# Performance work log

Measured on AMD Instinct MI355X. Metric: run time of the kernel, lower is better.

Reference implementation:

```python
import jax, jax.numpy as jnp
import numpy as np

D_MODEL = 256
NUM_HEADS = 8
CHUNK = 500
KEY_DIM = D_MODEL // NUM_HEADS      # 32
HEAD_DIM = KEY_DIM                  # value_factor = 1
SCALING = KEY_DIM ** -0.5
B, C, T = 2, 4, 2000                # T must be a multiple of CHUNK


def _rel_pos_constants(slen):
    # RetNetRelPos(chunkwise_recurrent=True)
    angle = 1.0 / (10000.0 ** jnp.linspace(0.0, 1.0, KEY_DIM // 2))
    angle = jnp.repeat(angle, 2)                                     # (KEY_DIM,)
    decay = jnp.log(1.0 - 2.0 ** (-5.0 - jnp.arange(NUM_HEADS, dtype=jnp.float32)))
    idx = jnp.arange(slen, dtype=jnp.float32)
    sin = jnp.sin(idx[:, None] * angle[None, :])                     # (T, KEY_DIM)
    cos = jnp.cos(idx[:, None] * angle[None, :])
    bi = jnp.arange(CHUNK, dtype=jnp.float32)
    diff = bi[:, None] - bi[None, :]
    mask = jnp.where(diff >= 0, jnp.exp(decay[:, None, None] * diff), 0.0)  # (H, cs, cs)
    last_row_sum = mask[:, -1].sum(-1)                               # (H,)
    value_inner_decay = (mask[:, -1] / last_row_sum[:, None])[:, :, None]   # (H, cs, 1)
    scale = jnp.sqrt(mask.sum(-1, keepdims=True))                    # (H, cs, 1)
    inner_mask = mask / scale
    cross_decay = jnp.exp(decay * CHUNK)[:, None, None]              # (H, 1, 1)
    qid = jnp.exp(decay[:, None] * (bi + 1.0))[:, :, None]           # (H, cs, 1)
    query_inner_decay = qid / (scale / last_row_sum[:, None, None])
    return sin, cos, inner_mask, cross_decay, query_inner_decay, value_inner_decay


def _rotate_every_two(x):
    x1, x2 = x[..., ::2], x[..., 1::2]
    return jnp.stack((-x2, x1), axis=-1).reshape(x.shape)


def _theta_shift(x, sin, cos):
    return x * cos + _rotate_every_two(x) * sin


def _layer_norm(x, g, b, eps=1e-5):
    mu = x.mean(-1, keepdims=True)
    var = ((x - mu) ** 2).mean(-1, keepdims=True)
    return (x - mu) * jax.lax.rsqrt(var + eps) * g + b


def _retention(x, qw, kw, vw, gw, ow):
    # MultiScaleRetention, chunkwise-recurrent mode
    bsz, t, _ = x.shape
    sin, cos, mask, cross_decay, q_decay, v_decay = _rel_pos_constants(t)
    q = x @ qw.T
    k = (x @ kw.T) * SCALING
    v = x @ vw.T
    g = x @ gw.T
    q = q.reshape(bsz, t, NUM_HEADS, KEY_DIM).transpose(0, 2, 1, 3)
    k = k.reshape(bsz, t, NUM_HEADS, KEY_DIM).transpose(0, 2, 1, 3)
    qr = _theta_shift(q, sin, cos)
    kr = _theta_shift(k, sin, cos)
    nc = t // CHUNK
    qr = qr.reshape(bsz, NUM_HEADS, nc, CHUNK, KEY_DIM).transpose(0, 2, 1, 3, 4)
    kr = kr.reshape(bsz, NUM_HEADS, nc, CHUNK, KEY_DIM).transpose(0, 2, 1, 3, 4)
    v = v.reshape(bsz, nc, CHUNK, NUM_HEADS, HEAD_DIM).transpose(0, 1, 3, 2, 4)
    qk = jnp.einsum('bnhik,bnhjk->bnhij', qr, kr) * mask             # (b,nc,h,cs,cs)
    inner_scale = jnp.maximum(jax.lax.stop_gradient(jnp.abs(qk)).sum(-1, keepdims=True), 1.0)
    inner_out = (qk / inner_scale) @ v                               # (b,nc,h,cs,hd)
    kv = jnp.einsum('bnhjk,bnhjd->bnhkd', kr, v * v_decay)           # (b,nc,h,kd,hd)

    def step(carry, kv_i):
        kv_state, kv_scale = carry
        out = (kv_state / kv_scale, kv_scale)
        kv_state = kv_state * cross_decay + kv_i
        kv_scale = jnp.maximum(
            jax.lax.stop_gradient(jnp.abs(kv_state)).sum(-2, keepdims=True).max(-1, keepdims=True), 1.0)
        return (kv_state, kv_scale), out

    init = (jnp.zeros((bsz, NUM_HEADS, KEY_DIM, HEAD_DIM), v.dtype),
            jnp.ones((bsz, NUM_HEADS, 1, 1), v.dtype))
    _, (kv_rec, cross_scale) = jax.lax.scan(step, init, jnp.moveaxis(kv, 1, 0))
    kv_rec = jnp.moveaxis(kv_rec, 0, 1)                              # (b,nc,h,kd,hd)
    cross_scale = jnp.moveaxis(cross_scale, 0, 1)                    # (b,nc,h,1,1)
    all_scale = jnp.maximum(inner_scale, cross_scale)
    cross_out = jnp.einsum('bnhik,bnhkd->bnhid', qr * q_decay, kv_rec)
    out = inner_out / (all_scale / inner_scale) + cross_out / (all_scale / cross_scale)
    out = out.transpose(0, 1, 3, 2, 4)                               # (b,nc,cs,h,hd)
    # group_norm = RMSNorm(head_dim, eps=1e-6, no affine)
    out = out * jax.lax.rsqrt(jnp.mean(out ** 2, -1, keepdims=True) + 1e-6)
    out = out.reshape(bsz, t, NUM_HEADS * HEAD_DIM)
    return (jax.nn.silu(g) * out) @ ow.T


def _mha(x, in_w, in_b, out_w, out_b):
    # torch.nn.MultiheadAttention, batch_first, eval (dropout off)
    bsz, s, _ = x.shape
    hd = D_MODEL // NUM_HEADS
    qkv = x @ in_w.T + in_b
    q, k, v = jnp.split(qkv, 3, axis=-1)
    q = q.reshape(bsz, s, NUM_HEADS, hd).transpose(0, 2, 1, 3) * (hd ** -0.5)
    k = k.reshape(bsz, s, NUM_HEADS, hd).transpose(0, 2, 1, 3)
    v = v.reshape(bsz, s, NUM_HEADS, hd).transpose(0, 2, 1, 3)
    attn = jax.nn.softmax(jnp.einsum('bhqd,bhkd->bhqk', q, k), axis=-1)
    out = jnp.einsum('bhqk,bhkd->bhqd', attn, v).transpose(0, 2, 1, 3).reshape(bsz, s, D_MODEL)
    return out @ out_w.T + out_b


def setup_inputs() -> dict:
    key = jax.random.key(0)
    ks = jax.random.split(key, 10)
    s = D_MODEL ** -0.5
    return {
        'inputs': jax.random.normal(ks[0], (B, C, T, D_MODEL), jnp.float32),
        'ln1_g': jnp.ones((D_MODEL,), jnp.float32),
        'ln1_b': jnp.zeros((D_MODEL,), jnp.float32),
        'ln2_g': jnp.ones((D_MODEL,), jnp.float32),
        'ln2_b': jnp.zeros((D_MODEL,), jnp.float32),
        'qw': jax.random.normal(ks[1], (D_MODEL, D_MODEL), jnp.float32) * s,
        'kw': jax.random.normal(ks[2], (D_MODEL, D_MODEL), jnp.float32) * s,
        'vw': jax.random.normal(ks[3], (D_MODEL, D_MODEL), jnp.float32) * s,
        'gw': jax.random.normal(ks[4], (D_MODEL, D_MODEL), jnp.float32) * s,
        'ow': jax.random.normal(ks[5], (D_MODEL, D_MODEL), jnp.float32) * s,
        'in_w': jax.random.normal(ks[6], (3 * D_MODEL, D_MODEL), jnp.float32) * s,
        'in_b': jnp.zeros((3 * D_MODEL,), jnp.float32),
        'out_w': jax.random.normal(ks[7], (D_MODEL, D_MODEL), jnp.float32) * s,
        'out_b': jnp.zeros((D_MODEL,), jnp.float32),
    }


def reference(inputs, ln1_g, ln1_b, ln2_g, ln2_b, qw, kw, vw, gw, ow, in_w, in_b, out_w, out_b):
    Bb, Cc, Tt, Dd = inputs.shape
    x = inputs.reshape(Bb * Cc, Tt, Dd)
    x = x + _retention(_layer_norm(x, ln1_g, ln1_b), qw, kw, vw, gw, ow)
    x = x.reshape(Bb, Cc, Tt, Dd).transpose(0, 2, 1, 3).reshape(Bb * Tt, Cc, Dd)
    x = x + _mha(_layer_norm(x, ln2_g, ln2_b), in_w, in_b, out_w, out_b)
    return x.reshape(Bb, Tt, Cc, Dd).transpose(0, 2, 1, 3)
```

## Files before the change

### kernel.cpp

```cpp
#include <hip/hip_runtime.h>
#include <math.h>

#define TLEN 2000
#define NSEQ 8
#define NHEADS 8
#define KD 32
#define CHUNKN 500
#define NCHUNK 4
#define MROWS 16000
#define SCALING 0.1767766952966369f

typedef float f32x4 __attribute__((ext_vector_type(4)));
typedef short s16x8 __attribute__((ext_vector_type(8)));
typedef unsigned short u16x8 __attribute__((ext_vector_type(8)));
typedef unsigned short u16x4 __attribute__((ext_vector_type(4)));

__device__ __forceinline__ unsigned short f2bf(float f) {
    unsigned int u = __float_as_uint(f);
    unsigned int r = (u + 0x7FFFu + ((u >> 16) & 1u)) >> 16;
    return (unsigned short)r;
}
__device__ __forceinline__ float bf2f(unsigned short h) {
    return __uint_as_float(((unsigned int)h) << 16);
}
__device__ __forceinline__ unsigned int cvtpk(float lo, float hi) {
    unsigned int r;
    asm("v_cvt_pk_bf16_f32 %0, %1, %2" : "=v"(r) : "v"(lo), "v"(hi));
    return r;
}

__global__ __launch_bounds__(256) void tab_kernel(float* __restrict__ sinT,
                                                  float* __restrict__ cosT) {
    int idx = blockIdx.x * 256 + threadIdx.x;
    if (idx >= TLEN * 16) return;
    int t = idx >> 4, a = idx & 15;
    float ang = powf(10000.0f, -(float)a / 15.0f);
    float th = (float)t * ang;
    sinT[idx] = sinf(th);
    cosT[idx] = cosf(th);
}

__global__ __launch_bounds__(256) void wcast_kernel(
    const float* __restrict__ qw, const float* __restrict__ kw,
    const float* __restrict__ vw, const float* __restrict__ gw,
    const float* __restrict__ ow, const float* __restrict__ inw,
    const float* __restrict__ outw, unsigned short* __restrict__ W) {
    int i = blockIdx.x * 1024 + threadIdx.x * 4;
    const float* src; int off;
    if (i < 65536)       { src = qw;   off = i; }
    else if (i < 131072) { src = kw;   off = i - 65536; }
    else if (i < 196608) { src = vw;   off = i - 131072; }
    else if (i < 262144) { src = gw;   off = i - 196608; }
    else if (i < 327680) { src = ow;   off = i - 262144; }
    else if (i < 524288) { src = inw;  off = i - 327680; }
    else                 { src = outw; off = i - 524288; }
    float4 v = *(const float4*)(src + off);
    u16x4 o;
    o[0] = f2bf(v.x); o[1] = f2bf(v.y); o[2] = f2bf(v.z); o[3] = f2bf(v.w);
    *(u16x4*)(W + i) = o;
}

__global__ __launch_bounds__(256) void ln_kernel(const float* __restrict__ x,
                                                 const float* __restrict__ gam,
                                                 const float* __restrict__ bet,
                                                 unsigned short* __restrict__ H,
                                                 unsigned short* __restrict__ L,
                                                 int rows) {
    int wid = threadIdx.x >> 6, lane = threadIdx.x & 63;
    int row = blockIdx.x * 4 + wid;
    if (row >= rows) return;
    const float* xr = x + (size_t)row * 256;
    float4 v = *(const float4*)(xr + lane * 4);
    float s = v.x + v.y + v.z + v.w;
    #pragma unroll
    for (int o = 32; o; o >>= 1) s += __shfl_xor(s, o);
    float mu = s * (1.0f / 256.0f);
    float dx = v.x - mu, dy = v.y - mu, dz = v.z - mu, dw = v.w - mu;
    float ss = dx * dx + dy * dy + dz * dz + dw * dw;
    #pragma unroll
    for (int o = 32; o; o >>= 1) ss += __shfl_xor(ss, o);
    float rstd = rsqrtf(ss * (1.0f / 256.0f) + 1e-5f);
    float4 g4 = *(const float4*)(gam + lane * 4);
    float4 b4 = *(const float4*)(bet + lane * 4);
    float ov[4];
    ov[0] = dx * rstd * g4.x + b4.x;
    ov[1] = dy * rstd * g4.y + b4.y;
    ov[2] = dz * rstd * g4.z + b4.z;
    ov[3] = dw * rstd * g4.w + b4.w;
    u16x4 hv, lv;
    #pragma unroll
    for (int j = 0; j < 4; ++j) {
        hv[j] = f2bf(ov[j]);
        lv[j] = f2bf(ov[j] - bf2f(hv[j]));
    }
    *(u16x4*)(H + (size_t)row * 256 + lane * 4) = hv;
    *(u16x4*)(L + (size_t)row * 256 + lane * 4) = lv;
}

template <int MODE>
__global__ __launch_bounds__(256, 2) void gemm_mfma(
    const unsigned short* __restrict__ AH, const unsigned short* __restrict__ AL,
    const unsigned short* __restrict__ Wc, const float* __restrict__ sinT,
    const float* __restrict__ cosT, const float* __restrict__ bias,
    const float* __restrict__ resid, float* __restrict__ D0,
    float* __restrict__ D1, float* __restrict__ D2, float* __restrict__ D3) {
    __shared__ unsigned short Ah[128][72];
    __shared__ unsigned short Al[128][72];
    __shared__ unsigned short Bt[128][72];
    const int tid = threadIdx.x;
    const int m0 = blockIdx.y * 128, n0 = blockIdx.x * 128;
    size_t wbase;
    if constexpr (MODE == 0)      wbase = (size_t)(n0 >> 8) * 65536 + (size_t)(n0 & 255) * 256;
    else if constexpr (MODE == 1) wbase = 262144 + (size_t)n0 * 256;
    else if constexpr (MODE == 2) wbase = 327680 + (size_t)n0 * 256;
    else                          wbase = 524288 + (size_t)n0 * 256;

    const int wid = tid >> 6, lane = tid & 63;
    const int wm = wid >> 1, wn = wid & 1;
    const int lr = lane & 15, lk = lane >> 4;
    const int str = tid >> 3;
    const int stc = (tid & 7) * 8;

    f32x4 acc[4][4] = {};

    for (int kt = 0; kt < 256; kt += 64) {
        if (kt) __syncthreads();
        #pragma unroll
        for (int it = 0; it < 4; ++it) {
            int r = it * 32 + str;
            u16x8 va = *(const u16x8*)(AH + (size_t)(m0 + r) * 256 + kt + stc);
            u16x8 vl = *(const u16x8*)(AL + (size_t)(m0 + r) * 256 + kt + stc);
            u16x8 vw = *(const u16x8*)(Wc + wbase + (size_t)r * 256 + kt + stc);
            *(u16x8*)(&Ah[r][stc]) = va;
            *(u16x8*)(&Al[r][stc]) = vl;
            *(u16x8*)(&Bt[r][stc]) = vw;
        }
        __syncthreads();
        #pragma unroll
        for (int ks = 0; ks < 2; ++ks) {
            const int k0 = ks * 32 + lk * 8;
            s16x8 af[4], alf[4], bf[4];
            #pragma unroll
            for (int f = 0; f < 4; ++f) {
                af[f]  = *(const s16x8*)(&Ah[wm * 64 + f * 16 + lr][k0]);
                alf[f] = *(const s16x8*)(&Al[wm * 64 + f * 16 + lr][k0]);
                bf[f]  = *(const s16x8*)(&Bt[wn * 64 + f * 16 + lr][k0]);
            }
            #pragma unroll
            for (int fm = 0; fm < 4; ++fm)
                #pragma unroll
                for (int fn = 0; fn < 4; ++fn) {
                    acc[fm][fn] = __builtin_amdgcn_mfma_f32_16x16x32_bf16(af[fm], bf[fn], acc[fm][fn], 0, 0, 0);
                    acc[fm][fn] = __builtin_amdgcn_mfma_f32_16x16x32_bf16(alf[fm], bf[fn], acc[fm][fn], 0, 0, 0);
                }
        }
    }

    if constexpr (MODE == 0) {
        const int w = n0 >> 8;
        const float sc = (w == 1) ? SCALING : 1.0f;
        #pragma unroll
        for (int fn = 0; fn < 4; ++fn) {
            const int c = n0 + wn * 64 + fn * 16 + lr;
            const int cb = c & 255, h = cb >> 5, d0 = cb & 31;
            #pragma unroll
            for (int fm = 0; fm < 4; ++fm)
                #pragma unroll
                for (int r = 0; r < 4; ++r) {
                    const int i = m0 + wm * 64 + fm * 16 + lk * 4 + r;
                    const int b = i / TLEN, t = i - b * TLEN;
                    float v = acc[fm][fn][r] * sc;
                    if (w <= 1) {
                        float oth = __shfl_xor(v, 1);
                        float cs = cosT[t * 16 + (d0 >> 1)];
                        float sn = sinT[t * 16 + (d0 >> 1)];
                        float outv = (d0 & 1) ? fmaf(v, cs, oth * sn) : fmaf(v, cs, -(oth * sn));
                        ((w == 0) ? D0 : D1)[((size_t)(b * NHEADS + h) * TLEN + t) * KD + d0] = outv;
                    } else if (w == 2) {
                        D2[((size_t)(b * NHEADS + h) * TLEN + t) * KD + d0] = v;
                    } else {
                        D3[(size_t)i * 256 + cb] = v;
                    }
                }
        }
    } else if constexpr (MODE == 1) {
        #pragma unroll
        for (int fn = 0; fn < 4; ++fn) {
            const int c = n0 + wn * 64 + fn * 16 + lr;
            #pragma unroll
            for (int fm = 0; fm < 4; ++fm)
                #pragma unroll
                for (int r = 0; r < 4; ++r) {
                    const int i = m0 + wm * 64 + fm * 16 + lk * 4 + r;
                    D0[(size_t)i * 256 + c] = resid[(size_t)i * 256 + c] + acc[fm][fn][r];
                }
        }
    } else if constexpr (MODE == 2) {
        const int w = n0 >> 8;
        const float qs = (w == 0) ? SCALING : 1.0f;
        float* Dsel = (w == 0) ? D0 : (w == 1) ? D1 : D2;
        #pragma unroll
        for (int fn = 0; fn < 4; ++fn) {
            const int c = n0 + wn * 64 + fn * 16 + lr;
            const int cb = c & 255;
            const float bv = bias[c];
            #pragma unroll
            for (int fm = 0; fm < 4; ++fm)
                #pragma unroll
                for (int r = 0; r < 4; ++r) {
                    const int i = m0 + wm * 64 + fm * 16 + lk * 4 + r;
                    Dsel[(size_t)i * 256 + cb] = (acc[fm][fn][r] + bv) * qs;
                }
        }
    } else {
        #pragma unroll
        for (int fn = 0; fn < 4; ++fn) {
            const int c = n0 + wn * 64 + fn * 16 + lr;
            const float bv = bias[c];
            #pragma unroll
            for (int fm = 0; fm < 4; ++fm)
                #pragma unroll
                for (int r = 0; r < 4; ++r) {
                    const int i = m0 + wm * 64 + fm * 16 + lk * 4 + r;
                    D0[(size_t)i * 256 + c] = resid[(size_t)i * 256 + c] + acc[fm][fn][r] + bv;
                }
        }
    }
}

__global__ __launch_bounds__(256) void kvp_kernel(const float* __restrict__ kr,
                                                  const float* __restrict__ v,
                                                  float* __restrict__ kvp) {
    int blk = blockIdx.x;
    int sub = blk & 1, rest = blk >> 1;
    int b = rest >> 5, n = (rest >> 3) & 3, h = rest & 7;
    int tid = threadIdx.x;
    int k = tid >> 3, d0 = (tid & 7) * 4;
    float dec = logf(1.0f - exp2f(-5.0f - (float)h));
    float lrs = (1.0f - expf(dec * (float)CHUNKN)) / (1.0f - expf(dec));
    float invl = 1.0f / lrs;
    const float* krb = kr + ((size_t)(b * NHEADS + h) * TLEN + n * CHUNKN) * KD;
    const float* vb = v + ((size_t)(b * NHEADS + h) * TLEN + n * CHUNKN) * KD;
    float a0 = 0, a1 = 0, a2 = 0, a3 = 0;
    int j0 = sub * 250;
    for (int j = j0; j < j0 + 250; ++j) {
        float kj = krb[(size_t)j * KD + k];
        float vd = expf(dec * (float)(CHUNKN - 1 - j)) * invl;
        float w = kj * vd;
        float4 vv = *(const float4*)(vb + (size_t)j * KD + d0);
        a0 = fmaf(w, vv.x, a0); a1 = fmaf(w, vv.y, a1);
        a2 = fmaf(w, vv.z, a2); a3 = fmaf(w, vv.w, a3);
    }
    float* dst = kvp + ((size_t)rest * 2 + sub) * 1024 + k * 32 + d0;
    dst[0] = a0; dst[1] = a1; dst[2] = a2; dst[3] = a3;
}

__global__ __launch_bounds__(256) void scan_kernel(const float* __restrict__ kvp,
                                                   float* __restrict__ rec,
                                                   float* __restrict__ sig) {
    __shared__ float cs[32];
    __shared__ float ssig;
    int blk = blockIdx.x;
    int b = blk >> 3, h = blk & 7;
    int tid = threadIdx.x;
    float dec = logf(1.0f - exp2f(-5.0f - (float)h));
    float cd = expf(dec * (float)CHUNKN);
    float S0 = 0, S1 = 0, S2 = 0, S3 = 0;
    float sigma = 1.0f;
    for (int n = 0; n < NCHUNK; ++n) {
        int rest = b * 32 + n * 8 + h;
        size_t rbase = (size_t)rest * 1024;
        size_t pbase = (size_t)rest * 2048;
        rec[rbase + tid] = S0;
        rec[rbase + tid + 256] = S1;
        rec[rbase + tid + 512] = S2;
        rec[rbase + tid + 768] = S3;
        if (tid == 0) sig[rest] = sigma;
        float k0 = 0, k1 = 0, k2 = 0, k3 = 0;
        #pragma unroll
        for (int s = 0; s < 2; ++s) {
            k0 += kvp[pbase + s * 1024 + tid];
            k1 += kvp[pbase + s * 1024 + tid + 256];
            k2 += kvp[pbase + s * 1024 + tid + 512];
            k3 += kvp[pbase + s * 1024 + tid + 768];
        }
        S0 = S0 * cd + k0;
        S1 = S1 * cd + k1;
        S2 = S2 * cd + k2;
        S3 = S3 * cd + k3;
        if (tid < 32) cs[tid] = 0.f;
        __syncthreads();
        float part = fabsf(S0) + fabsf(S1) + fabsf(S2) + fabsf(S3);
        atomicAdd(&cs[tid & 31], part);
        __syncthreads();
        if (tid == 0) {
            float m = cs[0];
            for (int d = 1; d < 32; ++d) m = fmaxf(m, cs[d]);
            ssig = fmaxf(m, 1.0f);
        }
        __syncthreads();
        sigma = ssig;
    }
}

__global__ __launch_bounds__(256, 2) void ret_core3(
    const float* __restrict__ qr, const float* __restrict__ kr,
    const float* __restrict__ v, const float* __restrict__ g,
    const float* __restrict__ rec, const float* __restrict__ sig,
    unsigned short* __restrict__ ABH, unsigned short* __restrict__ ABL) {
    __shared__ unsigned short Kt[64][40];
    __shared__ unsigned short Vt[32][72];
    __shared__ unsigned short SpH[32][40];
    __shared__ unsigned short SpL[32][40];
    __shared__ unsigned short Pl[128][72];

    const int u = 3 - (int)(blockIdx.x >> 8);
    const int chunk = blockIdx.x & 255;
    const int b = chunk >> 5, n = (chunk >> 3) & 3, h = chunk & 7;
    const int tid = threadIdx.x;
    const int wid = tid >> 6, lane = tid & 63;
    const int c = lane & 15, gq = lane >> 4;
    const float dec = logf(1.0f - exp2f(-5.0f - (float)h));
    const float ndec = -dec;
    const size_t cbase = ((size_t)(b * NHEADS + h) * TLEN + n * CHUNKN) * KD;
    const int i0 = u * 128 + wid * 32;
    const int NT = 2 * u + 2;
    const int jtmax_w = (i0 + 31) >> 6;

    s16x8 qh[2], ql[2];
    #pragma unroll
    for (int fi = 0; fi < 2; ++fi) {
        const float* qp = qr + cbase + (size_t)(i0 + fi * 16 + c) * KD + gq * 8;
        float4 a = *(const float4*)qp;
        float4 bq = *(const float4*)(qp + 4);
        float vals[8] = {a.x, a.y, a.z, a.w, bq.x, bq.y, bq.z, bq.w};
        u16x8 hv, lv;
        #pragma unroll
        for (int j = 0; j < 8; ++j) {
            hv[j] = f2bf(vals[j]);
            lv[j] = f2bf(vals[j] - bf2f(hv[j]));
        }
        qh[fi] = *(s16x8*)&hv;
        ql[fi] = *(s16x8*)&lv;
    }

    {
        int e0 = tid * 4;
        int k = e0 >> 5, d0 = e0 & 31;
        float4 sv = *(const float4*)(rec + (size_t)chunk * 1024 + e0);
        float se[4] = {sv.x, sv.y, sv.z, sv.w};
        #pragma unroll
        for (int j = 0; j < 4; ++j) {
            unsigned short hb = f2bf(se[j]);
            SpH[d0 + j][k] = hb;
            SpL[d0 + j][k] = f2bf(se[j] - bf2f(hb));
        }
    }

    f32x4 ot[2][2] = {};
    float absI[2] = {0.f, 0.f};

    for (int jt = 0; jt < NT; ++jt) {
        if (jt) __syncthreads();
        {
            int jl = tid >> 2, d0 = (tid & 3) * 8;
            int jg = jt * 64 + jl;
            float ej = expf(ndec * (float)jg);
            const float* kp = kr + cbase + (size_t)jg * KD + d0;
            const float* vp = v + cbase + (size_t)jg * KD + d0;
            float4 k0 = *(const float4*)kp, k1 = *(const float4*)(kp + 4);
            float4 v0 = *(const float4*)vp, v1 = *(const float4*)(vp + 4);
            u16x8 kb;
            kb[0] = f2bf(k0.x * ej); kb[1] = f2bf(k0.y * ej);
            kb[2] = f2bf(k0.z * ej); kb[3] = f2bf(k0.w * ej);
            kb[4] = f2bf(k1.x * ej); kb[5] = f2bf(k1.y * ej);
            kb[6] = f2bf(k1.z * ej); kb[7] = f2bf(k1.w * ej);
            *(u16x8*)&Kt[jl][d0] = kb;
            Vt[d0 + 0][jl] = f2bf(v0.x); Vt[d0 + 1][jl] = f2bf(v0.y);
            Vt[d0 + 2][jl] = f2bf(v0.z); Vt[d0 + 3][jl] = f2bf(v0.w);
            Vt[d0 + 4][jl] = f2bf(v1.x); Vt[d0 + 5][jl] = f2bf(v1.y);
            Vt[d0 + 6][jl] = f2bf(v1.z); Vt[d0 + 7][jl] = f2bf(v1.w);
        }
        __syncthreads();
        if (jt <= jtmax_w) {
            f32x4 st[4][2] = {};
            s16x8 ka[4];
            #pragma unroll
            for (int jf = 0; jf < 4; ++jf)
                ka[jf] = *(const s16x8*)&Kt[jf * 16 + c][gq * 8];
            #pragma unroll
            for (int jf = 0; jf < 4; ++jf)
                #pragma unroll
                for (int fi = 0; fi < 2; ++fi) {
                    st[jf][fi] = __builtin_amdgcn_mfma_f32_16x16x32_bf16(ka[jf], qh[fi], st[jf][fi], 0, 0, 0);
                    st[jf][fi] = __builtin_amdgcn_mfma_f32_16x16x32_bf16(ka[jf], ql[fi], st[jf][fi], 0, 0, 0);
                }
            const bool domask = (jt * 64 + 63 > i0);
            #pragma unroll
            for (int jf = 0; jf < 4; ++jf)
                #pragma unroll
                for (int fi = 0; fi < 2; ++fi) {
                    const int ii = i0 + fi * 16 + c;
                    if (domask) {
                        #pragma unroll
                        for (int r = 0; r < 4; ++r) {
                            int jg = jt * 64 + jf * 16 + gq * 4 + r;
                            if (jg > ii) st[jf][fi][r] = 0.f;
                        }
                    }
                    absI[fi] += (fabsf(st[jf][fi][0]) + fabsf(st[jf][fi][1])) +
                                (fabsf(st[jf][fi][2]) + fabsf(st[jf][fi][3]));
                    uint2 pw;
                    pw.x = cvtpk(st[jf][fi][0], st[jf][fi][1]);
                    pw.y = cvtpk(st[jf][fi][2], st[jf][fi][3]);
                    *(uint2*)&Pl[wid * 32 + fi * 16 + c][jf * 16 + gq * 4] = pw;
                }
            #pragma unroll
            for (int js = 0; js < 2; ++js) {
                s16x8 va0 = *(const s16x8*)&Vt[c][js * 32 + gq * 8];
                s16x8 va1 = *(const s16x8*)&Vt[16 + c][js * 32 + gq * 8];
                #pragma unroll
                for (int fi = 0; fi < 2; ++fi) {
                    s16x8 pb = *(const s16x8*)&Pl[wid * 32 + fi * 16 + c][js * 32 + gq * 8];
                    ot[0][fi] = __builtin_amdgcn_mfma_f32_16x16x32_bf16(va0, pb, ot[0][fi], 0, 0, 0);
                    ot[1][fi] = __builtin_amdgcn_mfma_f32_16x16x32_bf16(va1, pb, ot[1][fi], 0, 0, 0);
                }
            }
        }
    }

    f32x4 xt[2][2] = {};
    #pragma unroll
    for (int fd = 0; fd < 2; ++fd) {
        s16x8 sh = *(const s16x8*)&SpH[fd * 16 + c][gq * 8];
        s16x8 sl = *(const s16x8*)&SpL[fd * 16 + c][gq * 8];
        #pragma unroll
        for (int fi = 0; fi < 2; ++fi) {
            xt[fd][fi] = __builtin_amdgcn_mfma_f32_16x16x32_bf16(sh, qh[fi], xt[fd][fi], 0, 0, 0);
            xt[fd][fi] = __builtin_amdgcn_mfma_f32_16x16x32_bf16(sh, ql[fi], xt[fd][fi], 0, 0, 0);
            xt[fd][fi] = __builtin_amdgcn_mfma_f32_16x16x32_bf16(sl, qh[fi], xt[fd][fi], 0, 0, 0);
        }
    }

    const float er = expf(dec);
    const float inv1mr = 1.0f / (1.0f - er);
    const float lrs = (1.0f - expf(dec * (float)CHUNKN)) * inv1mr;
    const float sgp = sig[chunk];
    #pragma unroll
    for (int fi = 0; fi < 2; ++fi) {
        absI[fi] += __shfl_xor(absI[fi], 16);
        absI[fi] += __shfl_xor(absI[fi], 32);
        const int ii = i0 + fi * 16 + c;
        float rowsum = (1.0f - expf(dec * (float)(ii + 1))) * inv1mr;
        float iscale = rsqrtf(rowsum);
        float f_i = expf(dec * (float)ii) * iscale;
        float inner = fmaxf(absI[fi] * f_i, 1.0f);
        float alls = fmaxf(inner, sgp);
        float qd = expf(dec * (float)(ii + 1)) * lrs * iscale;
        float inva = 1.0f / alls;
        float vals[2][4];
        float ms = 0.f;
        #pragma unroll
        for (int fd = 0; fd < 2; ++fd)
            #pragma unroll
            for (int r = 0; r < 4; ++r) {
                float t = (ot[fd][fi][r] * f_i + xt[fd][fi][r] * qd) * inva;
                vals[fd][r] = t;
                ms += t * t;
            }
        ms += __shfl_xor(ms, 16);
        ms += __shfl_xor(ms, 32);
        float rn = rsqrtf(ms * (1.0f / 32.0f) + 1e-6f);
        const int tg = n * CHUNKN + ii;
        const float* gp = g + ((size_t)b * TLEN + tg) * 256 + h * KD;
        #pragma unroll
        for (int fd = 0; fd < 2; ++fd) {
            float4 gv = *(const float4*)(gp + fd * 16 + gq * 4);
            float ge[4] = {gv.x, gv.y, gv.z, gv.w};
            unsigned short hb[4], lb[4];
            #pragma unroll
            for (int r = 0; r < 4; ++r) {
                float sg = ge[r] / (1.0f + expf(-ge[r]));
                float ov = sg * vals[fd][r] * rn;
                hb[r] = f2bf(ov);
                lb[r] = f2bf(ov - bf2f(hb[r]));
            }
            uint2 ph, plw;
            ph.x = (unsigned int)hb[0] | ((unsigned int)hb[1] << 16);
            ph.y = (unsigned int)hb[2] | ((unsigned int)hb[3] << 16);
            plw.x = (unsigned int)lb[0] | ((unsigned int)lb[1] << 16);
            plw.y = (unsigned int)lb[2] | ((unsigned int)lb[3] << 16);
            *(uint2*)&Pl[wid * 32 + fi * 16 + c][fd * 16 + gq * 4] = ph;
            *(uint2*)&Pl[wid * 32 + fi * 16 + c][36 + fd * 16 + gq * 4] = plw;
        }
    }
    __syncthreads();
    {
        int r = tid & 127, half = tid >> 7;
        int ig = u * 128 + r;
        if (ig < CHUNKN) {
            unsigned short* D = half ? ABL : ABH;
            size_t dst = ((size_t)b * TLEN + n * CHUNKN + ig) * 256 + h * KD;
            #pragma unroll
            for (int k = 0; k < 4; ++k) {
                u16x4 a = *(const u16x4*)&Pl[r][half * 36 + k * 8];
                u16x4 bq = *(const u16x4*)&Pl[r][half * 36 + k * 8 + 4];
                u16x8 w;
                w[0] = a[0]; w[1] = a[1]; w[2] = a[2]; w[3] = a[3];
                w[4] = bq[0]; w[5] = bq[1]; w[6] = bq[2]; w[7] = bq[3];
                *(u16x8*)(D + dst + k * 8) = w;
            }
        }
    }
}

__global__ __launch_bounds__(256) void mha_attn(const float* __restrict__ qh,
                                                const float* __restrict__ kh,
                                                const float* __restrict__ vh,
                                                unsigned short* __restrict__ OH,
                                                unsigned short* __restrict__ OL) {
    int gidx = blockIdx.x * 256 + threadIdx.x;
    if (gidx >= 2 * TLEN * NHEADS * 4) return;
    int i = gidx & 3;
    int h = (gidx >> 2) & 7;
    int rest = gidx >> 5;
    int t = rest % TLEN;
    int b = rest / TLEN;
    size_t rows[4];
    #pragma unroll
    for (int c = 0; c < 4; ++c) rows[c] = ((size_t)(b * 4 + c) * TLEN + t);
    const float4* q4 = (const float4*)(qh + rows[i] * 256 + h * 32);
    float4 q[8];
    #pragma unroll
    for (int r = 0; r < 8; ++r) q[r] = q4[r];
    float s[4];
    #pragma unroll
    for (int j = 0; j < 4; ++j) {
        const float4* k4 = (const float4*)(kh + rows[j] * 256 + h * 32);
        float a0 = 0, a1 = 0, a2 = 0, a3 = 0;
        #pragma unroll
        for (int r = 0; r < 8; ++r) {
            float4 kk = k4[r];
            a0 = fmaf(q[r].x, kk.x, a0);
            a1 = fmaf(q[r].y, kk.y, a1);
            a2 = fmaf(q[r].z, kk.z, a2);
            a3 = fmaf(q[r].w, kk.w, a3);
        }
        s[j] = (a0 + a1) + (a2 + a3);
    }
    float m = fmaxf(fmaxf(s[0], s[1]), fmaxf(s[2], s[3]));
    float p[4], den = 0.f;
    #pragma unroll
    for (int j = 0; j < 4; ++j) { p[j] = expf(s[j] - m); den += p[j]; }
    float inv = 1.0f / den;
    float4 o[8];
    #pragma unroll
    for (int r = 0; r < 8; ++r) o[r] = make_float4(0.f, 0.f, 0.f, 0.f);
    #pragma unroll
    for (int j = 0; j < 4; ++j) {
        float wj = p[j] * inv;
        const float4* v4 = (const float4*)(vh + rows[j] * 256 + h * 32);
        #pragma unroll
        for (int r = 0; r < 8; ++r) {
            float4 vv = v4[r];
            o[r].x = fmaf(wj, vv.x, o[r].x);
            o[r].y = fmaf(wj, vv.y, o[r].y);
            o[r].z = fmaf(wj, vv.z, o[r].z);
            o[r].w = fmaf(wj, vv.w, o[r].w);
        }
    }
    #pragma unroll
    for (int r = 0; r < 8; ++r) {
        float vv[4] = {o[r].x, o[r].y, o[r].z, o[r].w};
        u16x4 hv, lv;
        #pragma unroll
        for (int j = 0; j < 4; ++j) {
            hv[j] = f2bf(vv[j]);
            lv[j] = f2bf(vv[j] - bf2f(hv[j]));
        }
        *(u16x4*)(OH + rows[i] * 256 + h * 32 + r * 4) = hv;
        *(u16x4*)(OL + rows[i] * 256 + h * 32 + r * 4) = lv;
    }
}

extern "C" void kernel_launch(void* const* d_in, const int* in_sizes, int n_in,
                              void* d_out, int out_size, void* d_ws, size_t ws_size,
                              hipStream_t stream) {
    (void)in_sizes; (void)n_in; (void)out_size; (void)ws_size;
    const float* x    = (const float*)d_in[0];
    const float* ln1g = (const float*)d_in[1];
    const float* ln1b = (const float*)d_in[2];
    const float* ln2g = (const float*)d_in[3];
    const float* ln2b = (const float*)d_in[4];
    const float* qw   = (const float*)d_in[5];
    const float* kw   = (const float*)d_in[6];
    const float* vw   = (const float*)d_in[7];
    const float* gw   = (const float*)d_in[8];
    const float* ow   = (const float*)d_in[9];
    const float* in_w = (const float*)d_in[10];
    const float* in_b = (const float*)d_in[11];
    const float* outw = (const float*)d_in[12];
    const float* outb = (const float*)d_in[13];
    float* out = (float*)d_out;
    float* ws = (float*)d_ws;

    constexpr size_t O_SIN = 0;
    constexpr size_t O_COS = 32000;
    constexpr size_t O_W   = 64000;
    constexpr size_t O_R1  = 358912;
    constexpr size_t O_R2  = O_R1 + 4096000;
    constexpr size_t O_R3  = O_R2 + 4096000;
    constexpr size_t O_R4  = O_R3 + 4096000;
    constexpr size_t O_H   = O_R4 + 4096000;
    constexpr size_t O_L   = O_H + 2048000;
    constexpr size_t O_REC = O_L + 2048000;
    constexpr size_t O_SIG = O_REC + 262144;

    float* sinT = ws + O_SIN;
    float* cosT = ws + O_COS;
    unsigned short* Wc = (unsigned short*)(ws + O_W);
    float* R1 = ws + O_R1;
    float* R2 = ws + O_R2;
    float* R3 = ws + O_R3;
    float* R4 = ws + O_R4;
    unsigned short* H = (unsigned short*)(ws + O_H);
    unsigned short* L = (unsigned short*)(ws + O_L);
    float* kvpf = ws + O_H;
    float* recb = ws + O_REC;
    float* sigb = ws + O_SIG;

    tab_kernel<<<125, 256, 0, stream>>>(sinT, cosT);
    wcast_kernel<<<576, 256, 0, stream>>>(qw, kw, vw, gw, ow, in_w, outw, Wc);
    ln_kernel<<<MROWS / 4, 256, 0, stream>>>(x, ln1g, ln1b, H, L, MROWS);
    gemm_mfma<0><<<dim3(8, 125), 256, 0, stream>>>(H, L, Wc, sinT, cosT, nullptr,
                                                   nullptr, R1, R2, R3, R4);
    kvp_kernel<<<512, 256, 0, stream>>>(R2, R3, kvpf);
    scan_kernel<<<64, 256, 0, stream>>>(kvpf, recb, sigb);
    ret_core3<<<1024, 256, 0, stream>>>(R1, R2, R3, R4, recb, sigb, H, L);
    gemm_mfma<1><<<dim3(2, 125), 256, 0, stream>>>(H, L, Wc, nullptr, nullptr,
                                                   nullptr, x, R1, nullptr, nullptr, nullptr);
    ln_kernel<<<MROWS / 4, 256, 0, stream>>>(R1, ln2g, ln2b, H, L, MROWS);
    gemm_mfma<2><<<dim3(6, 125), 256, 0, stream>>>(H, L, Wc, nullptr, nullptr,
                                                   in_b, nullptr, R2, R3, R4, nullptr);
    mha_attn<<<500, 256, 0, stream>>>(R2, R3, R4, H, L);
    gemm_mfma<3><<<dim3(2, 125), 256, 0, stream>>>(H, L, Wc, nullptr, nullptr,
                                                   outb, R1, out, nullptr, nullptr, nullptr);
}
```

Before: 281.9 us.

## Store intermediate projections as bf16 via LDS-staged coalesced epilogue writes

The QKV/G projection GEMM and the MHA in-projection GEMM now write bf16 instead of fp32. Q is stored as a hi/lo bf16 pair, and K, V, G and the MHA q/k/v are stored as single bf16. The epilogue stages each tile through shared memory so stores are coalesced 16-byte writes. The downstream retention, kvp and MHA kernels read bf16 directly, which removes per-element conversion work and halves intermediate memory traffic. The cost is reduced precision for K, V, G and the MHA inputs (previously fp32) and extra syncs in the epilogue.

New measurement: 271.1 us. -3.9%, faster.

```diff
diff --git a/kernel.cpp b/kernel.cpp
--- a/kernel.cpp
+++ b/kernel.cpp
@@ -102,8 +102,10 @@
     const unsigned short* __restrict__ AH, const unsigned short* __restrict__ AL,
     const unsigned short* __restrict__ Wc, const float* __restrict__ sinT,
     const float* __restrict__ cosT, const float* __restrict__ bias,
-    const float* __restrict__ resid, float* __restrict__ D0,
-    float* __restrict__ D1, float* __restrict__ D2, float* __restrict__ D3) {
+    const float* __restrict__ resid, float* __restrict__ F0,
+    unsigned short* __restrict__ U0, unsigned short* __restrict__ U1,
+    unsigned short* __restrict__ U2, unsigned short* __restrict__ U3,
+    unsigned short* __restrict__ U4) {
     __shared__ unsigned short Ah[128][72];
     __shared__ unsigned short Al[128][72];
     __shared__ unsigned short Bt[128][72];
@@ -158,61 +160,80 @@
 
     if constexpr (MODE == 0) {
         const int w = n0 >> 8;
-        const float sc = (w == 1) ? SCALING : 1.0f;
+        if (w <= 1) {
+            const float sc = (w == 1) ? SCALING : 1.0f;
+            #pragma unroll
+            for (int fn = 0; fn < 4; ++fn) {
+                const int c = n0 + wn * 64 + fn * 16 + lr;
+                const int d0 = c & 31;
+                #pragma unroll
+                for (int fm = 0; fm < 4; ++fm)
+                    #pragma unroll
+                    for (int r = 0; r < 4; ++r) {
+                        const int i = m0 + wm * 64 + fm * 16 + lk * 4 + r;
+                        const int t = i % TLEN;
+                        float vraw = acc[fm][fn][r] * sc;
+                        float oth = __shfl_xor(vraw, 1);
+                        float cs = cosT[t * 16 + (d0 >> 1)];
+                        float sn = sinT[t * 16 + (d0 >> 1)];
+                        acc[fm][fn][r] = (d0 & 1) ? fmaf(vraw, cs, oth * sn)
+                                                  : fmaf(vraw, cs, -(oth * sn));
+                    }
+            }
+        }
+        unsigned short* Dsel = (w == 0) ? U0 : (w == 1) ? U2 : (w == 2) ? U3 : U4;
+        for (int half = 0; half < 2; ++half) {
+            const int np = (w == 0) ? 2 : 1;
+            for (int pass = 0; pass < np; ++pass) {
+                __syncthreads();
+                if (wn == half) {
+                    #pragma unroll
+                    for (int fn = 0; fn < 4; ++fn)
+                        #pragma unroll
+                        for (int fm = 0; fm < 4; ++fm)
+                            #pragma unroll
+                            for (int r = 0; r < 4; ++r) {
+                                float x = acc[fm][fn][r];
+                                unsigned short hb = f2bf(x);
+                                unsigned short ob = pass ? f2bf(x - bf2f(hb)) : hb;
+                                Ah[wm * 64 + fm * 16 + lk * 4 + r][fn * 16 + lr] = ob;
+                            }
+                }
+                __syncthreads();
+                unsigned short* D = (w == 0 && pass) ? U1 : Dsel;
+                #pragma unroll
+                for (int it = 0; it < 4; ++it) {
+                    int flat = it * 2048 + tid * 8;
+                    int r = flat >> 6, cl = flat & 63;
+                    u16x8 val = *(const u16x8*)&Ah[r][cl];
+                    int i = m0 + r;
+                    int cb = (n0 & 255) + half * 64 + cl;
+                    if (w <= 2) {
+                        int bb = i / TLEN, t = i - bb * TLEN;
+                        int hh = cb >> 5, d0 = cb & 31;
+                        *(u16x8*)(D + ((size_t)(bb * NHEADS + hh) * TLEN + t) * KD + d0) = val;
+                    } else {
+                        *(u16x8*)(D + (size_t)i * 256 + cb) = val;
+                    }
+                }
+            }
+        }
+    } else if constexpr (MODE == 1) {
         #pragma unroll
         for (int fn = 0; fn < 4; ++fn) {
             const int c = n0 + wn * 64 + fn * 16 + lr;
-            const int cb = c & 255, h = cb >> 5, d0 = cb & 31;
             #pragma unroll
             for (int fm = 0; fm < 4; ++fm)
                 #pragma unroll
                 for (int r = 0; r < 4; ++r) {
                     const int i = m0 + wm * 64 + fm * 16 + lk * 4 + r;
-                    const int b = i / TLEN, t = i - b * TLEN;
-                    float v = acc[fm][fn][r] * sc;
-                    if (w <= 1) {
-                        float oth = __shfl_xor(v, 1);
-                        float cs = cosT[t * 16 + (d0 >> 1)];
-                        float sn = sinT[t * 16 + (d0 >> 1)];
-                        float outv = (d0 & 1) ? fmaf(v, cs, oth * sn) : fmaf(v, cs, -(oth * sn));
-                        ((w == 0) ? D0 : D1)[((size_t)(b * NHEADS + h) * TLEN + t) * KD + d0] = outv;
-                    } else if (w == 2) {
-                        D2[((size_t)(b * NHEADS + h) * TLEN + t) * KD + d0] = v;
-                    } else {
-                        D3[(size_t)i * 256 + cb] = v;
-                    }
-                }
-        }
-    } else if constexpr (MODE == 1) {
-        #pragma unroll
-        for (int fn = 0; fn < 4; ++fn) {
-            const int c = n0 + wn * 64 + fn * 16 + lr;
-            #pragma unroll
-            for (int fm = 0; fm < 4; ++fm)
-                #pragma unroll
-                for (int r = 0; r < 4; ++r) {
-                    const int i = m0 + wm * 64 + fm * 16 + lk * 4 + r;
-                    D0[(size_t)i * 256 + c] = resid[(size_t)i * 256 + c] + acc[fm][fn][r];
+                    F0[(size_t)i * 256 + c] = resid[(size_t)i * 256 + c] + acc[fm][fn][r];
                 }
         }
     } else if constexpr (MODE == 2) {
         const int w = n0 >> 8;
         const float qs = (w == 0) ? SCALING : 1.0f;
-        float* Dsel = (w == 0) ? D0 : (w == 1) ? D1 : D2;
-        #pragma unroll
-        for (int fn = 0; fn < 4; ++fn) {
-            const int c = n0 + wn * 64 + fn * 16 + lr;
-            const int cb = c & 255;
-            const float bv = bias[c];
-            #pragma unroll
-            for (int fm = 0; fm < 4; ++fm)
-                #pragma unroll
-                for (int r = 0; r < 4; ++r) {
-                    const int i = m0 + wm * 64 + fm * 16 + lk * 4 + r;
-                    Dsel[(size_t)i * 256 + cb] = (acc[fm][fn][r] + bv) * qs;
-                }
-        }
-    } else {
+        unsigned short* Dsel = (w == 0) ? U0 : (w == 1) ? U1 : U2;
         #pragma unroll
         for (int fn = 0; fn < 4; ++fn) {
             const int c = n0 + wn * 64 + fn * 16 + lr;
@@ -220,16 +241,50 @@
             #pragma unroll
             for (int fm = 0; fm < 4; ++fm)
                 #pragma unroll
+                for (int r = 0; r < 4; ++r)
+                    acc[fm][fn][r] = (acc[fm][fn][r] + bv) * qs;
+        }
+        for (int half = 0; half < 2; ++half) {
+            __syncthreads();
+            if (wn == half) {
+                #pragma unroll
+                for (int fn = 0; fn < 4; ++fn)
+                    #pragma unroll
+                    for (int fm = 0; fm < 4; ++fm)
+                        #pragma unroll
+                        for (int r = 0; r < 4; ++r)
+                            Ah[wm * 64 + fm * 16 + lk * 4 + r][fn * 16 + lr] =
+                                f2bf(acc[fm][fn][r]);
+            }
+            __syncthreads();
+            #pragma unroll
+            for (int it = 0; it < 4; ++it) {
+                int flat = it * 2048 + tid * 8;
+                int r = flat >> 6, cl = flat & 63;
+                u16x8 val = *(const u16x8*)&Ah[r][cl];
+                int i = m0 + r;
+                int cb = (n0 & 255) + half * 64 + cl;
+                *(u16x8*)(Dsel + (size_t)i * 256 + cb) = val;
+            }
+        }
+    } else {
+        #pragma unroll
+        for (int fn = 0; fn < 4; ++fn) {
+            const int c = n0 + wn * 64 + fn * 16 + lr;
+            const float bv = bias[c];
+            #pragma unroll
+            for (int fm = 0; fm < 4; ++fm)
+                #pragma unroll
                 for (int r = 0; r < 4; ++r) {
                     const int i = m0 + wm * 64 + fm * 16 + lk * 4 + r;
-                    D0[(size_t)i * 256 + c] = resid[(size_t)i * 256 + c] + acc[fm][fn][r] + bv;
+                    F0[(size_t)i * 256 + c] = resid[(size_t)i * 256 + c] + acc[fm][fn][r] + bv;
                 }
         }
     }
 }
 
-__global__ __launch_bounds__(256) void kvp_kernel(const float* __restrict__ kr,
-                                                  const float* __restrict__ v,
+__global__ __launch_bounds__(256) void kvp_kernel(const unsigned short* __restrict__ KB,
+                                                  const unsigned short* __restrict__ VB,
                                                   float* __restrict__ kvp) {
     int blk = blockIdx.x;
     int sub = blk & 1, rest = blk >> 1;
@@ -239,17 +294,17 @@
     float dec = logf(1.0f - exp2f(-5.0f - (float)h));
     float lrs = (1.0f - expf(dec * (float)CHUNKN)) / (1.0f - expf(dec));
     float invl = 1.0f / lrs;
-    const float* krb = kr + ((size_t)(b * NHEADS + h) * TLEN + n * CHUNKN) * KD;
-    const float* vb = v + ((size_t)(b * NHEADS + h) * TLEN + n * CHUNKN) * KD;
+    const unsigned short* krb = KB + ((size_t)(b * NHEADS + h) * TLEN + n * CHUNKN) * KD;
+    const unsigned short* vb = VB + ((size_t)(b * NHEADS + h) * TLEN + n * CHUNKN) * KD;
     float a0 = 0, a1 = 0, a2 = 0, a3 = 0;
     int j0 = sub * 250;
     for (int j = j0; j < j0 + 250; ++j) {
-        float kj = krb[(size_t)j * KD + k];
+        float kj = bf2f(krb[(size_t)j * KD + k]);
         float vd = expf(dec * (float)(CHUNKN - 1 - j)) * invl;
         float w = kj * vd;
-        float4 vv = *(const float4*)(vb + (size_t)j * KD + d0);
-        a0 = fmaf(w, vv.x, a0); a1 = fmaf(w, vv.y, a1);
-        a2 = fmaf(w, vv.z, a2); a3 = fmaf(w, vv.w, a3);
+        u16x4 vv = *(const u16x4*)(vb + (size_t)j * KD + d0);
+        a0 = fmaf(w, bf2f(vv[0]), a0); a1 = fmaf(w, bf2f(vv[1]), a1);
+        a2 = fmaf(w, bf2f(vv[2]), a2); a3 = fmaf(w, bf2f(vv[3]), a3);
     }
     float* dst = kvp + ((size_t)rest * 2 + sub) * 1024 + k * 32 + d0;
     dst[0] = a0; dst[1] = a1; dst[2] = a2; dst[3] = a3;
@@ -304,8 +359,9 @@
 }
 
 __global__ __launch_bounds__(256, 2) void ret_core3(
-    const float* __restrict__ qr, const float* __restrict__ kr,
-    const float* __restrict__ v, const float* __restrict__ g,
+    const unsigned short* __restrict__ QH, const unsigned short* __restrict__ QL,
+    const unsigned short* __restrict__ KB, const unsigned short* __restrict__ VB,
+    const unsigned short* __restrict__ GB,
     const float* __restrict__ rec, const float* __restrict__ sig,
     unsigned short* __restrict__ ABH, unsigned short* __restrict__ ABL) {
     __shared__ unsigned short Kt[64][40];
@@ -322,7 +378,7 @@
     const int c = lane & 15, gq = lane >> 4;
     const float dec = logf(1.0f - exp2f(-5.0f - (float)h));
     const float ndec = -dec;
-    const size_t cbase = ((size_t)(b * NHEADS + h) * TLEN + n * CHUNKN) * KD;
+    const size_t cb16 = ((size_t)(b * NHEADS + h) * TLEN + n * CHUNKN) * KD;
     const int i0 = u * 128 + wid * 32;
     const int NT = 2 * u + 2;
     const int jtmax_w = (i0 + 31) >> 6;
@@ -330,18 +386,9 @@
     s16x8 qh[2], ql[2];
     #pragma unroll
     for (int fi = 0; fi < 2; ++fi) {
-        const float* qp = qr + cbase + (size_t)(i0 + fi * 16 + c) * KD + gq * 8;
-        float4 a = *(const float4*)qp;
-        float4 bq = *(const float4*)(qp + 4);
-        float vals[8] = {a.x, a.y, a.z, a.w, bq.x, bq.y, bq.z, bq.w};
-        u16x8 hv, lv;
-        #pragma unroll
-        for (int j = 0; j < 8; ++j) {
-            hv[j] = f2bf(vals[j]);
-            lv[j] = f2bf(vals[j] - bf2f(hv[j]));
-        }
-        qh[fi] = *(s16x8*)&hv;
-        ql[fi] = *(s16x8*)&lv;
+        size_t off = cb16 + (size_t)(i0 + fi * 16 + c) * KD + gq * 8;
+        qh[fi] = *(const s16x8*)(QH + off);
+        ql[fi] = *(const s16x8*)(QL + off);
     }
 
     {
@@ -366,20 +413,14 @@
             int jl = tid >> 2, d0 = (tid & 3) * 8;
             int jg = jt * 64 + jl;
             float ej = expf(ndec * (float)jg);
-            const float* kp = kr + cbase + (size_t)jg * KD + d0;
-            const float* vp = v + cbase + (size_t)jg * KD + d0;
-            float4 k0 = *(const float4*)kp, k1 = *(const float4*)(kp + 4);
-            float4 v0 = *(const float4*)vp, v1 = *(const float4*)(vp + 4);
+            u16x8 kraw = *(const u16x8*)(KB + cb16 + (size_t)jg * KD + d0);
+            u16x8 vraw = *(const u16x8*)(VB + cb16 + (size_t)jg * KD + d0);
             u16x8 kb;
-            kb[0] = f2bf(k0.x * ej); kb[1] = f2bf(k0.y * ej);
-            kb[2] = f2bf(k0.z * ej); kb[3] = f2bf(k0.w * ej);
-            kb[4] = f2bf(k1.x * ej); kb[5] = f2bf(k1.y * ej);
-            kb[6] = f2bf(k1.z * ej); kb[7] = f2bf(k1.w * ej);
+            #pragma unroll
+            for (int e = 0; e < 8; ++e) kb[e] = f2bf(bf2f(kraw[e]) * ej);
             *(u16x8*)&Kt[jl][d0] = kb;
-            Vt[d0 + 0][jl] = f2bf(v0.x); Vt[d0 + 1][jl] = f2bf(v0.y);
-            Vt[d0 + 2][jl] = f2bf(v0.z); Vt[d0 + 3][jl] = f2bf(v0.w);
-            Vt[d0 + 4][jl] = f2bf(v1.x); Vt[d0 + 5][jl] = f2bf(v1.y);
-            Vt[d0 + 6][jl] = f2bf(v1.z); Vt[d0 + 7][jl] = f2bf(v1.w);
+            #pragma unroll
+            for (int e = 0; e < 8; ++e) Vt[d0 + e][jl] = vraw[e];
         }
         __syncthreads();
         if (jt <= jtmax_w) {
@@ -472,15 +513,15 @@
         ms += __shfl_xor(ms, 32);
         float rn = rsqrtf(ms * (1.0f / 32.0f) + 1e-6f);
         const int tg = n * CHUNKN + ii;
-        const float* gp = g + ((size_t)b * TLEN + tg) * 256 + h * KD;
+        const unsigned short* gp = GB + ((size_t)b * TLEN + tg) * 256 + h * KD;
         #pragma unroll
         for (int fd = 0; fd < 2; ++fd) {
-            float4 gv = *(const float4*)(gp + fd * 16 + gq * 4);
-            float ge[4] = {gv.x, gv.y, gv.z, gv.w};
+            u16x4 gv = *(const u16x4*)(gp + fd * 16 + gq * 4);
             unsigned short hb[4], lb[4];
             #pragma unroll
             for (int r = 0; r < 4; ++r) {
-                float sg = ge[r] / (1.0f + expf(-ge[r]));
+                float ge = bf2f(gv[r]);
+                float sg = ge / (1.0f + expf(-ge));
                 float ov = sg * vals[fd][r] * rn;
                 hb[r] = f2bf(ov);
                 lb[r] = f2bf(ov - bf2f(hb[r]));
@@ -514,9 +555,9 @@
     }
 }
 
-__global__ __launch_bounds__(256) void mha_attn(const float* __restrict__ qh,
-                                                const float* __restrict__ kh,
-                                                const float* __restrict__ vh,
+__global__ __launch_bounds__(256) void mha_attn(const unsigned short* __restrict__ qh_,
+                                                const unsigned short* __restrict__ kh_,
+                                                const unsigned short* __restrict__ vh_,
                                                 unsigned short* __restrict__ OH,
                                                 unsigned short* __restrict__ OL) {
     int gidx = blockIdx.x * 256 + threadIdx.x;
@@ -529,22 +570,29 @@
     size_t rows[4];
     #pragma unroll
     for (int c = 0; c < 4; ++c) rows[c] = ((size_t)(b * 4 + c) * TLEN + t);
-    const float4* q4 = (const float4*)(qh + rows[i] * 256 + h * 32);
-    float4 q[8];
-    #pragma unroll
-    for (int r = 0; r < 8; ++r) q[r] = q4[r];
+    float q[32];
+    #pragma unroll
+    for (int rb = 0; rb < 4; ++rb) {
+        u16x8 t8 = *(const u16x8*)(qh_ + rows[i] * 256 + h * 32 + rb * 8);
+        #pragma unroll
+        for (int e = 0; e < 8; ++e) q[rb * 8 + e] = bf2f(t8[e]);
+    }
     float s[4];
     #pragma unroll
     for (int j = 0; j < 4; ++j) {
-        const float4* k4 = (const float4*)(kh + rows[j] * 256 + h * 32);
+        const unsigned short* kp = kh_ + rows[j] * 256 + h * 32;
         float a0 = 0, a1 = 0, a2 = 0, a3 = 0;
         #pragma unroll
-        for (int r = 0; r < 8; ++r) {
-            float4 kk = k4[r];
-            a0 = fmaf(q[r].x, kk.x, a0);
-            a1 = fmaf(q[r].y, kk.y, a1);
-            a2 = fmaf(q[r].z, kk.z, a2);
-            a3 = fmaf(q[r].w, kk.w, a3);
+        for (int rb = 0; rb < 4; ++rb) {
+            u16x8 t8 = *(const u16x8*)(kp + rb * 8);
+            a0 = fmaf(q[rb * 8 + 0], bf2f(t8[0]), a0);
+            a1 = fmaf(q[rb * 8 + 1], bf2f(t8[1]), a1);
+            a2 = fmaf(q[rb * 8 + 2], bf2f(t8[2]), a2);
+            a3 = fmaf(q[rb * 8 + 3], bf2f(t8[3]), a3);
+            a0 = fmaf(q[rb * 8 + 4], bf2f(t8[4]), a0);
+            a1 = fmaf(q[rb * 8 + 5], bf2f(t8[5]), a1);
+            a2 = fmaf(q[rb * 8 + 6], bf2f(t8[6]), a2);
+            a3 = fmaf(q[rb * 8 + 7], bf2f(t8[7]), a3);
         }
         s[j] = (a0 + a1) + (a2 + a3);
     }
@@ -553,33 +601,32 @@
     #pragma unroll
     for (int j = 0; j < 4; ++j) { p[j] = expf(s[j] - m); den += p[j]; }
     float inv = 1.0f / den;
-    float4 o[8];
-    #pragma unroll
-    for (int r = 0; r < 8; ++r) o[r] = make_float4(0.f, 0.f, 0.f, 0.f);
+    float o[32];
+    #pragma unroll
+    for (int e = 0; e < 32; ++e) o[e] = 0.f;
     #pragma unroll
     for (int j = 0; j < 4; ++j) {
         float wj = p[j] * inv;
-        const float4* v4 = (const float4*)(vh + rows[j] * 256 + h * 32);
-        #pragma unroll
-        for (int r = 0; r < 8; ++r) {
-            float4 vv = v4[r];
-            o[r].x = fmaf(wj, vv.x, o[r].x);
-            o[r].y = fmaf(wj, vv.y, o[r].y);
-            o[r].z = fmaf(wj, vv.z, o[r].z);
-            o[r].w = fmaf(wj, vv.w, o[r].w);
-        }
-    }
-    #pragma unroll
-    for (int r = 0; r < 8; ++r) {
-        float vv[4] = {o[r].x, o[r].y, o[r].z, o[r].w};
+        const unsigned short* vp = vh_ + rows[j] * 256 + h * 32;
+        #pragma unroll
+        for (int rb = 0; rb < 4; ++rb) {
+            u16x8 t8 = *(const u16x8*)(vp + rb * 8);
+            #pragma unroll
+            for (int e = 0; e < 8; ++e)
+                o[rb * 8 + e] = fmaf(wj, bf2f(t8[e]), o[rb * 8 + e]);
+        }
+    }
+    #pragma unroll
+    for (int rb = 0; rb < 8; ++rb) {
         u16x4 hv, lv;
         #pragma unroll
-        for (int j = 0; j < 4; ++j) {
-            hv[j] = f2bf(vv[j]);
-            lv[j] = f2bf(vv[j] - bf2f(hv[j]));
-        }
-        *(u16x4*)(OH + rows[i] * 256 + h * 32 + r * 4) = hv;
-        *(u16x4*)(OL + rows[i] * 256 + h * 32 + r * 4) = lv;
+        for (int e = 0; e < 4; ++e) {
+            float x = o[rb * 4 + e];
+            hv[e] = f2bf(x);
+            lv[e] = f2bf(x - bf2f(hv[e]));
+        }
+        *(u16x4*)(OH + rows[i] * 256 + h * 32 + rb * 4) = hv;
+        *(u16x4*)(OL + rows[i] * 256 + h * 32 + rb * 4) = lv;
     }
 }
 
@@ -607,11 +654,12 @@
     constexpr size_t O_SIN = 0;
     constexpr size_t O_COS = 32000;
     constexpr size_t O_W   = 64000;
-    constexpr size_t O_R1  = 358912;
-    constexpr size_t O_R2  = O_R1 + 4096000;
-    constexpr size_t O_R3  = O_R2 + 4096000;
-    constexpr size_t O_R4  = O_R3 + 4096000;
-    constexpr size_t O_H   = O_R4 + 4096000;
+    constexpr size_t O_QH  = 358912;
+    constexpr size_t O_QL  = O_QH + 2048000;
+    constexpr size_t O_KB  = O_QL + 2048000;
+    constexpr size_t O_VB  = O_KB + 2048000;
+    constexpr size_t O_GB  = O_VB + 2048000;
+    constexpr size_t O_H   = O_GB + 2048000;
     constexpr size_t O_L   = O_H + 2048000;
     constexpr size_t O_REC = O_L + 2048000;
     constexpr size_t O_SIG = O_REC + 262144;
@@ -619,12 +667,17 @@
     float* sinT = ws + O_SIN;
     float* cosT = ws + O_COS;
     unsigned short* Wc = (unsigned short*)(ws + O_W);
-    float* R1 = ws + O_R1;
-    float* R2 = ws + O_R2;
-    float* R3 = ws + O_R3;
-    float* R4 = ws + O_R4;
-    unsigned short* H = (unsigned short*)(ws + O_H);
-    unsigned short* L = (unsigned short*)(ws + O_L);
+    unsigned short* QH = (unsigned short*)(ws + O_QH);
+    unsigned short* QL = (unsigned short*)(ws + O_QL);
+    unsigned short* KB = (unsigned short*)(ws + O_KB);
+    unsigned short* VB = (unsigned short*)(ws + O_VB);
+    unsigned short* GB = (unsigned short*)(ws + O_GB);
+    unsigned short* H  = (unsigned short*)(ws + O_H);
+    unsigned short* L  = (unsigned short*)(ws + O_L);
+    float* x2   = ws + O_QH;
+    unsigned short* qhat = KB;
+    unsigned short* khat = VB;
+    unsigned short* vhat = GB;
     float* kvpf = ws + O_H;
     float* recb = ws + O_REC;
     float* sigb = ws + O_SIG;
@@ -633,16 +686,19 @@
     wcast_kernel<<<576, 256, 0, stream>>>(qw, kw, vw, gw, ow, in_w, outw, Wc);
     ln_kernel<<<MROWS / 4, 256, 0, stream>>>(x, ln1g, ln1b, H, L, MROWS);
     gemm_mfma<0><<<dim3(8, 125), 256, 0, stream>>>(H, L, Wc, sinT, cosT, nullptr,
-                                                   nullptr, R1, R2, R3, R4);
-    kvp_kernel<<<512, 256, 0, stream>>>(R2, R3, kvpf);
+                                                   nullptr, nullptr, QH, QL, KB, VB, GB);
+    kvp_kernel<<<512, 256, 0, stream>>>(KB, VB, kvpf);
     scan_kernel<<<64, 256, 0, stream>>>(kvpf, recb, sigb);
-    ret_core3<<<1024, 256, 0, stream>>>(R1, R2, R3, R4, recb, sigb, H, L);
+    ret_core3<<<1024, 256, 0, stream>>>(QH, QL, KB, VB, GB, recb, sigb, H, L);
     gemm_mfma<1><<<dim3(2, 125), 256, 0, stream>>>(H, L, Wc, nullptr, nullptr,
-                                                   nullptr, x, R1, nullptr, nullptr, nullptr);
-    ln_kernel<<<MROWS / 4, 256, 0, stream>>>(R1, ln2g, ln2b, H, L, MROWS);
+                                                   nullptr, x, x2,
+                                                   nullptr, nullptr, nullptr, nullptr, nullptr);
+    ln_kernel<<<MROWS / 4, 256, 0, stream>>>(x2, ln2g, ln2b, H, L, MROWS);
     gemm_mfma<2><<<dim3(6, 125), 256, 0, stream>>>(H, L, Wc, nullptr, nullptr,
-                                                   in_b, nullptr, R2, R3, R4, nullptr);
-    mha_attn<<<500, 256, 0, stream>>>(R2, R3, R4, H, L);
+                                                   in_b, nullptr, nullptr,
+                                                   qhat, khat, vhat, nullptr, nullptr);
+    mha_attn<<<500, 256, 0, stream>>>(qhat, khat, vhat, H, L);
     gemm_mfma<3><<<dim3(2, 125), 256, 0, stream>>>(H, L, Wc, nullptr, nullptr,
-                                                   outb, R1, out, nullptr, nullptr, nullptr);
-}
+                                                   outb, x2, out,
+                                                   nullptr, nullptr, nullptr, nullptr, nullptr);
+}
```
